# Performance work log

Hardware: AMD Instinct MI355X
Metric: run time of the kernel (lower is better)

## Reference

```python
import jax, jax.numpy as jnp
import numpy as np

IN_F, OUT_F, RANK = 4096, 4096, 8
TOKENS = 8192


def setup_inputs() -> dict:
    key = jax.random.key(0)
    k1, k2, k3 = jax.random.split(key, 3)
    x = jax.random.normal(k1, (TOKENS, IN_F), dtype=jnp.float32)
    # xavier-uniform-ish init scale for the TT cores
    lim0 = float(np.sqrt(6.0 / (OUT_F + RANK)))
    lim1 = float(np.sqrt(6.0 / (RANK + IN_F)))
    core0 = jax.random.uniform(k2, (1, OUT_F, RANK), minval=-lim0, maxval=lim0, dtype=jnp.float32)
    core1 = jax.random.uniform(k3, (RANK, IN_F, 1), minval=-lim1, maxval=lim1, dtype=jnp.float32)
    bias = jnp.zeros((OUT_F,), dtype=jnp.float32)
    return {"x": x, "core0": core0, "core1": core1, "bias": bias}


def reference(x, core0, core1, bias):
    # Faithful to torch: weight[o, i] = sum_r core0[0, o, r] * core1[r, i, 0]
    # (original einsum 'ior, ri1 -> oi' with the size-1 leading/trailing dims broadcast)
    weight = jnp.einsum('or,ri->oi', core0[0], core1[:, :, 0])  # [OUT_F, IN_F]
    # F.linear: x @ weight.T + bias
    return x @ weight.T + bias
```

## Files before the change

### kernel.cpp

```cpp
#include <hip/hip_runtime.h>


#define TOKENS 8192
#define IN_F   4096
#define OUT_F  4096
#define RANK   8

__global__ __launch_bounds__(256) void tt_phase1(const float* __restrict__ x,
                                                 const float* __restrict__ core1,
                                                 float* __restrict__ y) {
    const int tid  = threadIdx.x;
    const int wave = tid >> 6;
    const int lane = tid & 63;
    const int t0   = blockIdx.x * 8 + wave * 2;

    const float* x0 = x + (size_t)t0 * IN_F;
    const float* x1 = x0 + IN_F;

    float acc0[RANK], acc1[RANK];
    #pragma unroll
    for (int r = 0; r < RANK; ++r) { acc0[r] = 0.f; acc1[r] = 0.f; }

    #pragma unroll 4
    for (int k = 0; k < 16; ++k) {
        const int i = 4 * (lane + 64 * k);
        const float4 a0 = *(const float4*)(x0 + i);
        const float4 a1 = *(const float4*)(x1 + i);
        #pragma unroll
        for (int r = 0; r < RANK; ++r) {
            const float4 c = *(const float4*)(core1 + r * IN_F + i);
            acc0[r] += a0.x * c.x + a0.y * c.y + a0.z * c.z + a0.w * c.w;
            acc1[r] += a1.x * c.x + a1.y * c.y + a1.z * c.z + a1.w * c.w;
        }
    }

    #pragma unroll
    for (int r = 0; r < RANK; ++r) {
        #pragma unroll
        for (int off = 32; off > 0; off >>= 1) {
            acc0[r] += __shfl_xor(acc0[r], off, 64);
            acc1[r] += __shfl_xor(acc1[r], off, 64);
        }
    }

    if (lane == 0) {
        float4* yp = (float4*)(y + (size_t)t0 * RANK);
        yp[0] = make_float4(acc0[0], acc0[1], acc0[2], acc0[3]);
        yp[1] = make_float4(acc0[4], acc0[5], acc0[6], acc0[7]);
        yp[2] = make_float4(acc1[0], acc1[1], acc1[2], acc1[3]);
        yp[3] = make_float4(acc1[4], acc1[5], acc1[6], acc1[7]);
    }
}

__global__ __launch_bounds__(256) void tt_phase2(const float* __restrict__ y,
                                                 const float* __restrict__ core0,
                                                 const float* __restrict__ bias,
                                                 float* __restrict__ out) {
    const int og    = blockIdx.x & 3;
    const int tg    = blockIdx.x >> 2;
    const int o     = og * 1024 + threadIdx.x * 4;
    const int tbase = tg * 32;

    float4 w[8];
    #pragma unroll
    for (int j = 0; j < 4; ++j) {
        w[2 * j]     = *(const float4*)(core0 + (o + j) * RANK);
        w[2 * j + 1] = *(const float4*)(core0 + (o + j) * RANK + 4);
    }
    const float4 b = *(const float4*)(bias + o);

    #pragma unroll 4
    for (int tt = 0; tt < 32; ++tt) {
        const int t = tbase + tt;
        const float4 y0 = *(const float4*)(y + t * RANK);
        const float4 y1 = *(const float4*)(y + t * RANK + 4);
        float4 c;
        c.x = b.x + y0.x * w[0].x + y0.y * w[0].y + y0.z * w[0].z + y0.w * w[0].w
                  + y1.x * w[1].x + y1.y * w[1].y + y1.z * w[1].z + y1.w * w[1].w;
        c.y = b.y + y0.x * w[2].x + y0.y * w[2].y + y0.z * w[2].z + y0.w * w[2].w
                  + y1.x * w[3].x + y1.y * w[3].y + y1.z * w[3].z + y1.w * w[3].w;
        c.z = b.z + y0.x * w[4].x + y0.y * w[4].y + y0.z * w[4].z + y0.w * w[4].w
                  + y1.x * w[5].x + y1.y * w[5].y + y1.z * w[5].z + y1.w * w[5].w;
        c.w = b.w + y0.x * w[6].x + y0.y * w[6].y + y0.z * w[6].z + y0.w * w[6].w
                  + y1.x * w[7].x + y1.y * w[7].y + y1.z * w[7].z + y1.w * w[7].w;
        *(float4*)(out + (size_t)t * OUT_F + o) = c;
    }
}

extern "C" void kernel_launch(void* const* d_in, const int* in_sizes, int n_in,
                              void* d_out, int out_size, void* d_ws, size_t ws_size,
                              hipStream_t stream) {
    const float* x     = (const float*)d_in[0];
    const float* core0 = (const float*)d_in[1];
    const float* core1 = (const float*)d_in[2];
    const float* bias  = (const float*)d_in[3];
    float* out = (float*)d_out;
    float* y   = (float*)d_ws;

    tt_phase1<<<TOKENS / 8, 256, 0, stream>>>(x, core1, y);
    tt_phase2<<<(OUT_F / 1024) * (TOKENS / 32), 256, 0, stream>>>(y, core0, bias, out);
}
```

Before: 275.8 us.

## Fuse TT projection phases into one kernel via shared-memory intermediate

Merges the rank-projection and expansion kernels into a single kernel. Each block computes the 8-rank projections for 8 tokens, stores them in shared memory, syncs, then writes the full output rows for those tokens. This removes the second launch and the global round trip of the intermediate. In exchange each block reloads core0 and bias for all outputs, and the write phase is serialized behind the reduction within each block.

New measurement: 280.5 us. No clear change (+1.7%).

```diff
diff --git a/kernel.cpp b/kernel.cpp
--- a/kernel.cpp
+++ b/kernel.cpp
@@ -6,15 +6,19 @@
 #define OUT_F  4096
 #define RANK   8
 
-__global__ __launch_bounds__(256) void tt_phase1(const float* __restrict__ x,
-                                                 const float* __restrict__ core1,
-                                                 float* __restrict__ y) {
+__global__ __launch_bounds__(256) void tt_fused(const float* __restrict__ x,
+                                                const float* __restrict__ core0,
+                                                const float* __restrict__ core1,
+                                                const float* __restrict__ bias,
+                                                float* __restrict__ out) {
+    __shared__ float y_s[8][RANK];
+
     const int tid  = threadIdx.x;
     const int wave = tid >> 6;
     const int lane = tid & 63;
-    const int t0   = blockIdx.x * 8 + wave * 2;
+    const int t0   = blockIdx.x * 8;
 
-    const float* x0 = x + (size_t)t0 * IN_F;
+    const float* x0 = x + (size_t)(t0 + wave * 2) * IN_F;
     const float* x1 = x0 + IN_F;
 
     float acc0[RANK], acc1[RANK];
@@ -44,46 +48,41 @@
     }
 
     if (lane == 0) {
-        float4* yp = (float4*)(y + (size_t)t0 * RANK);
-        yp[0] = make_float4(acc0[0], acc0[1], acc0[2], acc0[3]);
-        yp[1] = make_float4(acc0[4], acc0[5], acc0[6], acc0[7]);
-        yp[2] = make_float4(acc1[0], acc1[1], acc1[2], acc1[3]);
-        yp[3] = make_float4(acc1[4], acc1[5], acc1[6], acc1[7]);
+        #pragma unroll
+        for (int r = 0; r < RANK; ++r) {
+            y_s[wave * 2][r]     = acc0[r];
+            y_s[wave * 2 + 1][r] = acc1[r];
+        }
     }
-}
+    __syncthreads();
 
-__global__ __launch_bounds__(256) void tt_phase2(const float* __restrict__ y,
-                                                 const float* __restrict__ core0,
-                                                 const float* __restrict__ bias,
-                                                 float* __restrict__ out) {
-    const int og    = blockIdx.x & 3;
-    const int tg    = blockIdx.x >> 2;
-    const int o     = og * 1024 + threadIdx.x * 4;
-    const int tbase = tg * 32;
-
-    float4 w[8];
     #pragma unroll
     for (int j = 0; j < 4; ++j) {
-        w[2 * j]     = *(const float4*)(core0 + (o + j) * RANK);
-        w[2 * j + 1] = *(const float4*)(core0 + (o + j) * RANK + 4);
-    }
-    const float4 b = *(const float4*)(bias + o);
+        const int o = j * 1024 + tid * 4;
 
-    #pragma unroll 4
-    for (int tt = 0; tt < 32; ++tt) {
-        const int t = tbase + tt;
-        const float4 y0 = *(const float4*)(y + t * RANK);
-        const float4 y1 = *(const float4*)(y + t * RANK + 4);
-        float4 c;
-        c.x = b.x + y0.x * w[0].x + y0.y * w[0].y + y0.z * w[0].z + y0.w * w[0].w
-                  + y1.x * w[1].x + y1.y * w[1].y + y1.z * w[1].z + y1.w * w[1].w;
-        c.y = b.y + y0.x * w[2].x + y0.y * w[2].y + y0.z * w[2].z + y0.w * w[2].w
-                  + y1.x * w[3].x + y1.y * w[3].y + y1.z * w[3].z + y1.w * w[3].w;
-        c.z = b.z + y0.x * w[4].x + y0.y * w[4].y + y0.z * w[4].z + y0.w * w[4].w
-                  + y1.x * w[5].x + y1.y * w[5].y + y1.z * w[5].z + y1.w * w[5].w;
-        c.w = b.w + y0.x * w[6].x + y0.y * w[6].y + y0.z * w[6].z + y0.w * w[6].w
-                  + y1.x * w[7].x + y1.y * w[7].y + y1.z * w[7].z + y1.w * w[7].w;
-        *(float4*)(out + (size_t)t * OUT_F + o) = c;
+        float4 w[8];
+        #pragma unroll
+        for (int q = 0; q < 4; ++q) {
+            w[2 * q]     = *(const float4*)(core0 + (o + q) * RANK);
+            w[2 * q + 1] = *(const float4*)(core0 + (o + q) * RANK + 4);
+        }
+        const float4 b = *(const float4*)(bias + o);
+
+        #pragma unroll
+        for (int t = 0; t < 8; ++t) {
+            const float4 y0 = *(const float4*)(&y_s[t][0]);
+            const float4 y1 = *(const float4*)(&y_s[t][4]);
+            float4 c;
+            c.x = b.x + y0.x * w[0].x + y0.y * w[0].y + y0.z * w[0].z + y0.w * w[0].w
+                      + y1.x * w[1].x + y1.y * w[1].y + y1.z * w[1].z + y1.w * w[1].w;
+            c.y = b.y + y0.x * w[2].x + y0.y * w[2].y + y0.z * w[2].z + y0.w * w[2].w
+                      + y1.x * w[3].x + y1.y * w[3].y + y1.z * w[3].z + y1.w * w[3].w;
+            c.z = b.z + y0.x * w[4].x + y0.y * w[4].y + y0.z * w[4].z + y0.w * w[4].w
+                      + y1.x * w[5].x + y1.y * w[5].y + y1.z * w[5].z + y1.w * w[5].w;
+            c.w = b.w + y0.x * w[6].x + y0.y * w[6].y + y0.z * w[6].z + y0.w * w[6].w
+                      + y1.x * w[7].x + y1.y * w[7].y + y1.z * w[7].z + y1.w * w[7].w;
+            *(float4*)(out + (size_t)(t0 + t) * OUT_F + o) = c;
+        }
     }
 }
 
@@ -95,8 +94,6 @@
     const float* core1 = (const float*)d_in[2];
     const float* bias  = (const float*)d_in[3];
     float* out = (float*)d_out;
-    float* y   = (float*)d_ws;
 
-    tt_phase1<<<TOKENS / 8, 256, 0, stream>>>(x, core1, y);
-    tt_phase2<<<(OUT_F / 1024) * (TOKENS / 32), 256, 0, stream>>>(y, core0, bias, out);
+    tt_fused<<<TOKENS / 8, 256, 0, stream>>>(x, core0, core1, bias, out);
 }
```
